# Kernel tuning notes

Hardware: AMD Instinct MI355X
Metric: run time of the kernel (lower is better)

The kernel has to match this reference:

```python
import jax, jax.numpy as jnp
import numpy as np
from jax import lax

NUM_HOP = 2      # opt.num_hop
POOL_HOP = 1     # Encoder(..., num_hop=1) in gnn_pools
K_POOL = 1024    # int(pooling_ratio * num_patches) = 0.5 * 2048
TH = 0.0         # opt.nonzero_th
T = 0.07         # NCE temperature
NEG_FILL = -10.0


def l2norm(x):
    # Normalize(power=2): x / (sum(x^2, dim=1, keepdim)^(1/2))
    return x / jnp.sqrt(jnp.sum(x * x, axis=1, keepdims=True))


def tagconv(A, h, W, b, k):
    # DGL TAGConv: concat_{i=0..k} (D^-1/2 A D^-1/2)^i h, then linear
    deg = jnp.sum(A, axis=1)
    dinv = lax.rsqrt(jnp.maximum(deg, 1e-12))
    An = A * dinv[:, None] * dinv[None, :]   # [N,N] normalized adjacency
    feats = [h]
    for _ in range(k):
        h = An @ h
        feats.append(h)
    return jnp.concatenate(feats, axis=1) @ W + b


def nce_pair(f_t, f_s):
    # calc_gnn NCE: positives = diag(f_t . f_s); negatives = full gram with diag masked to -10
    n = f_t.shape[0]
    eye = jnp.eye(n, dtype=bool)
    pos = jnp.sum(f_t * f_s, axis=1, keepdims=True)          # [N,1]
    neg_s = jnp.where(eye, NEG_FILL, f_t @ f_s.T)            # [N,N]
    neg_t = jnp.where(eye, NEG_FILL, f_s @ f_t.T)
    out_s = jnp.concatenate([pos, neg_s], axis=1) / T
    out_t = jnp.concatenate([pos, neg_t], axis=1) / T
    # CrossEntropy with label 0 == -log_softmax(out)[:, 0], mean over rows
    loss_s = -jnp.mean(jax.nn.log_softmax(out_s, axis=1)[:, 0])
    loss_t = -jnp.mean(jax.nn.log_softmax(out_t, axis=1)[:, 0])
    return loss_s + loss_t


def setup_inputs() -> dict:
    key = jax.random.key(0)
    ks = jax.random.split(key, 8)
    N, C, D = 2048, 512, 128
    g = 0.02  # init_gain ('normal' init)
    return {
        "fs": jax.random.normal(ks[0], (N, C), jnp.float32),
        "ft": jax.random.normal(ks[1], (N, C), jnp.float32),
        "W_embed": g * jax.random.normal(ks[2], (C, D), jnp.float32),
        "b_embed": jnp.zeros((D,), jnp.float32),
        "W_gnn": g * jax.random.normal(ks[3], ((NUM_HOP + 1) * D, D), jnp.float32),
        "b_gnn": jnp.zeros((D,), jnp.float32),
        "W_pool": g * jax.random.normal(ks[4], (D, 1), jnp.float32),
        "b_pool": jnp.zeros((1,), jnp.float32),
        "W_gnnp": g * jax.random.normal(ks[5], ((POOL_HOP + 1) * D, D), jnp.float32),
        "b_gnnp": jnp.zeros((D,), jnp.float32),
    }


def reference(fs, ft, W_embed, b_embed, W_gnn, b_gnn, W_pool, b_pool, W_gnnp, b_gnnp):
    # Embed: linear + l2 norm
    f_es = l2norm(fs @ W_embed + b_embed)   # student [N, nc]
    f_et = l2norm(ft @ W_embed + b_embed)   # teacher [N, nc]

    # nonzero_graph on detached teacher features; same adjacency reused for student
    ft_d = lax.stop_gradient(f_et)
    n = f_et.shape[0]
    eye = jnp.eye(n, dtype=bool)
    A = (ft_d @ ft_d.T > TH).astype(f_et.dtype)
    A = jnp.where(eye, 1.0, A)  # dgl.add_self_loop

    # TAGConv encoder + l2norm; teacher branch detached
    f_gt = lax.stop_gradient(l2norm(tagconv(A, f_et, W_gnn, b_gnn, NUM_HOP)))
    f_gs = l2norm(tagconv(A, f_es, W_gnn, b_gnn, NUM_HOP))
    loss_g = nce_pair(f_gt, f_gs)

    # Pool / top_k_graph
    scores = jax.nn.sigmoid((f_gt @ W_pool + b_pool)[:, 0])   # [N]
    vals, idx = lax.top_k(scores, K_POOL)
    new_ht = f_gt[idx] * vals[:, None]
    new_hs = f_gs[idx] * vals[:, None]
    un = (A > 0).astype(A.dtype)
    un2 = ((un @ un) > 0).astype(A.dtype)        # 2-hop boolean adjacency
    sub = un2[idx][:, idx]                       # [k,k]
    deg = jnp.sum(sub, axis=1)
    g_pool = sub / deg[None, :]                  # replicates torch broadcast in norm_g(g/degrees)

    # pooled-stage Encoder (TAGConv k=1) on the pooled graph structure (with self loops)
    k = K_POOL
    eye_k = jnp.eye(k, dtype=bool)
    Ap = (g_pool > 0).astype(A.dtype)
    Ap = jnp.where(eye_k, 1.0, Ap)
    f_pt = lax.stop_gradient(l2norm(tagconv(Ap, new_ht, W_gnnp, b_gnnp, POOL_HOP)))
    f_ps = l2norm(tagconv(Ap, new_hs, W_gnnp, b_gnnp, POOL_HOP))
    loss_pool = nce_pair(f_pt, f_ps)

    return loss_g + loss_pool
```

## Files before the change

### kernel.cpp

```cpp
#include <hip/hip_runtime.h>


#define TINV (1.0f / 0.07f)

using short8 = __attribute__((ext_vector_type(8))) short;
using f32x4  = __attribute__((ext_vector_type(4))) float;

__device__ __forceinline__ unsigned short f2bf(float f) {
    unsigned u = __float_as_uint(f);
    u += 0x7fff + ((u >> 16) & 1);
    return (unsigned short)(u >> 16);
}

template<bool BT>
__device__ __forceinline__ void mm_tile(const float* __restrict__ A, int lda,
                                        const float* __restrict__ B, int ldb,
                                        int i0, int j0, int k0, int k1,
                                        float (&acc)[4][4],
                                        float (&As)[16][68], float (&Bs)[16][68])
{
    const int tid = threadIdx.x;
    const int tx = tid & 15;
    const int ty = tid >> 4;
    const int lr = tid >> 2;
    const int lc = (tid & 3) * 4;
    for (int k = k0; k < k1; k += 16) {
        float4 av = *(const float4*)(A + (size_t)(i0 + lr) * lda + (k + lc));
        As[lc + 0][lr] = av.x; As[lc + 1][lr] = av.y;
        As[lc + 2][lr] = av.z; As[lc + 3][lr] = av.w;
        if (BT) {
            float4 bv = *(const float4*)(B + (size_t)(j0 + lr) * ldb + (k + lc));
            Bs[lc + 0][lr] = bv.x; Bs[lc + 1][lr] = bv.y;
            Bs[lc + 2][lr] = bv.z; Bs[lc + 3][lr] = bv.w;
        } else {
            const int n = tid & 63;
            const int kb = tid >> 6;
#pragma unroll
            for (int it = 0; it < 4; ++it)
                Bs[kb * 4 + it][n] = B[(size_t)(k + kb * 4 + it) * ldb + (j0 + n)];
        }
        __syncthreads();
#pragma unroll
        for (int kk = 0; kk < 16; ++kk) {
            float a[4], b[4];
#pragma unroll
            for (int u = 0; u < 4; ++u) a[u] = As[kk][ty * 4 + u];
#pragma unroll
            for (int v = 0; v < 4; ++v) b[v] = Bs[kk][tx * 4 + v];
#pragma unroll
            for (int u = 0; u < 4; ++u)
#pragma unroll
                for (int v = 0; v < 4; ++v)
                    acc[u][v] = fmaf(a[u], b[v], acc[u][v]);
        }
        __syncthreads();
    }
}

__device__ __forceinline__ void mm64x128(const unsigned short* __restrict__ Ab, int lda,
                                         const unsigned short* __restrict__ Bb, int ldb,
                                         int i0, int j0, int k0, int Kc,
                                         f32x4 (&acc)[8],
                                         unsigned short (&As)[64][40],
                                         unsigned short (&Bs)[128][40])
{
    const int tid = threadIdx.x;
    const int w = tid >> 6;
    const int lane = tid & 63;
    const int m = lane & 15;
    const int q = lane >> 4;
    const int ar = tid >> 2;
    const int ac = (tid & 3) * 8;
    for (int ks = 0; ks < Kc; ks += 32) {
        const int k = k0 + ks;
        *(ulonglong2*)&As[ar][ac] =
            *(const ulonglong2*)(Ab + (size_t)(i0 + ar) * lda + k + ac);
        *(ulonglong2*)&Bs[ar][ac] =
            *(const ulonglong2*)(Bb + (size_t)(j0 + ar) * ldb + k + ac);
        *(ulonglong2*)&Bs[ar + 64][ac] =
            *(const ulonglong2*)(Bb + (size_t)(j0 + ar + 64) * ldb + k + ac);
        __syncthreads();
        short8 a = *(const short8*)&As[w * 16 + m][q * 8];
#pragma unroll
        for (int nt = 0; nt < 8; ++nt) {
            short8 b = *(const short8*)&Bs[nt * 16 + m][q * 8];
            acc[nt] = __builtin_amdgcn_mfma_f32_16x16x32_bf16(a, b, acc[nt], 0, 0, 0);
        }
        __syncthreads();
    }
}

__launch_bounds__(256)
__global__ void k_setup_embed(const float* __restrict__ fs, const float* __restrict__ ft,
                              const float* __restrict__ W, float* __restrict__ part,
                              size_t zstr, int* __restrict__ zwords, int zcount,
                              float* __restrict__ out,
                              const float* __restrict__ Wg, const float* __restrict__ Wp,
                              unsigned short* __restrict__ Wtall)
{
    __shared__ float As[16][68];
    __shared__ float Bs[16][68];
    const int b = blockIdx.x;
    const int tid = threadIdx.x;
    if (b < 512) {
        const int z = b & 3;
        const int by = (b >> 2) & 63;
        const int bx = b >> 8;
        const float* A = (by < 32) ? ft : fs;
        const int i0 = (by & 31) * 64;
        const int j0 = bx * 64;
        float acc[4][4] = {};
        mm_tile<false>(A, 512, W, 128, i0, j0, z * 128, z * 128 + 128, acc, As, Bs);
        const int tx = tid & 15, ty = tid >> 4;
        float* dst = part + (size_t)z * zstr;
#pragma unroll
        for (int u = 0; u < 4; ++u) {
            const size_t ri = (size_t)(by * 64 + ty * 4 + u) * 128 + j0 + tx * 4;
            float4 vv;
            vv.x = acc[u][0]; vv.y = acc[u][1]; vv.z = acc[u][2]; vv.w = acc[u][3];
            *(float4*)(dst + ri) = vv;
        }
    } else if (b < 561) {
        const int i = (b - 512) * 256 + tid;
        if (i < zcount) zwords[i] = 0;
        if (b == 512 && tid == 0) out[0] = 0.0f;
    } else {
        const int e0 = (b - 561) * 2048 + tid;
#pragma unroll
        for (int it = 0; it < 8; ++it) {
            const int e = e0 + it * 256;
            const int c = e >> 14;
            const int rem = e & 16383;
            const int n = rem >> 7, k = rem & 127;
            const float* src = (c < 3) ? (Wg + (size_t)c * 16384)
                                       : (Wp + (size_t)(c - 3) * 16384);
            Wtall[e] = f2bf(src[(size_t)k * 128 + n]);
        }
    }
}

__global__ void combine_norm(const float* __restrict__ part, int nz, size_t zstr,
                             const float* __restrict__ bias,
                             float* __restrict__ f32out,
                             unsigned short* __restrict__ bf16out)
{
    const int row = blockIdx.x;
    const int tid = threadIdx.x;
    float v = bias[tid];
    for (int z = 0; z < nz; ++z) v += part[(size_t)z * zstr + (size_t)row * 128 + tid];
    __shared__ float red[128];
    red[tid] = v * v;
    __syncthreads();
    for (int s = 64; s > 0; s >>= 1) {
        if (tid < s) red[tid] += red[tid + s];
        __syncthreads();
    }
    const float o = v * (1.0f / sqrtf(red[0]));
    f32out[(size_t)row * 128 + tid] = o;
    bf16out[(size_t)row * 128 + tid] = f2bf(o);
}

__launch_bounds__(256)
__global__ void k_gram_fused(const float* __restrict__ f_e,
                             unsigned short* __restrict__ A01,
                             unsigned long long* __restrict__ bits,
                             int* __restrict__ deg,
                             const unsigned short* __restrict__ feb,
                             const unsigned short* __restrict__ Wt,
                             float* __restrict__ hW)
{
    __shared__ __align__(16) unsigned char smem[15360];
    const int b = blockIdx.x;
    const int tid = threadIdx.x;
    if (b >= 528) {
        unsigned short (&As2)[64][40]  = *reinterpret_cast<unsigned short(*)[64][40]>(smem);
        unsigned short (&Bs2)[128][40] = *reinterpret_cast<unsigned short(*)[128][40]>(smem + 5120);
        const int lb = b - 528;
        const int z = lb >> 6;
        const int i0 = (lb & 63) * 64;
        f32x4 acc[8];
#pragma unroll
        for (int t = 0; t < 8; ++t)
#pragma unroll
            for (int r = 0; r < 4; ++r) acc[t][r] = 0.0f;
        mm64x128(feb, 128, Wt + (size_t)z * 16384, 128, i0, 0, 0, 128, acc, As2, Bs2);
        const int w = tid >> 6, lane = tid & 63, m = lane & 15, q = lane >> 4;
        float* Cb = hW + (size_t)z * (4096ull * 128);
#pragma unroll
        for (int nt = 0; nt < 8; ++nt) {
            const int col = nt * 16 + m;
#pragma unroll
            for (int r = 0; r < 4; ++r) {
                const int row = i0 + w * 16 + q * 4 + r;
                Cb[(size_t)row * 128 + col] = acc[nt][r];
            }
        }
        return;
    }
    float (&As)[16][68] = *reinterpret_cast<float(*)[16][68]>(smem);
    float (&Bs)[16][68] = *reinterpret_cast<float(*)[16][68]>(smem + 4352);
    unsigned char (&nib)[64][16]  = *reinterpret_cast<unsigned char(*)[64][16]>(smem + 8704);
    unsigned char (&nibT)[64][16] = *reinterpret_cast<unsigned char(*)[64][16]>(smem + 9728);
    unsigned long long (&chk)[64]  = *reinterpret_cast<unsigned long long(*)[64]>(smem + 10752);
    unsigned long long (&chkT)[64] = *reinterpret_cast<unsigned long long(*)[64]>(smem + 11264);
    int by = (int)((sqrtf(8.0f * b + 1.0f) - 1.0f) * 0.5f);
    while ((by + 1) * (by + 2) / 2 <= b) ++by;
    while (by * (by + 1) / 2 > b) --by;
    const int bx = b - by * (by + 1) / 2;
    const int i0 = by * 64, j0 = bx * 64;
    float acc[4][4] = {};
    mm_tile<true>(f_e, 128, f_e, 128, i0, j0, 0, 128, acc, As, Bs);
    const int tx = tid & 15, ty = tid >> 4;
    unsigned pb = 0;
#pragma unroll
    for (int u = 0; u < 4; ++u)
#pragma unroll
        for (int v = 0; v < 4; ++v) {
            bool pred = (acc[u][v] > 0.0f) || (i0 + ty * 4 + u == j0 + tx * 4 + v);
            pb |= (unsigned)pred << (u * 4 + v);
        }
#pragma unroll
    for (int u = 0; u < 4; ++u) nib[ty * 4 + u][tx] = (pb >> (4 * u)) & 15;
#pragma unroll
    for (int v = 0; v < 4; ++v) {
        unsigned nt = 0;
#pragma unroll
        for (int u = 0; u < 4; ++u) nt |= ((pb >> (u * 4 + v)) & 1u) << u;
        nibT[tx * 4 + v][ty] = nt;
    }
    __syncthreads();
    if (tid < 64) {
        unsigned long long c = 0;
#pragma unroll
        for (int t = 0; t < 16; ++t) c |= (unsigned long long)nib[tid][t] << (4 * t);
        chk[tid] = c;
        bits[(size_t)(i0 + tid) * 32 + (j0 >> 6)] = c;
        atomicAdd(&deg[i0 + tid], __popcll(c));
    } else if (tid < 128 && bx != by) {
        const int r = tid - 64;
        unsigned long long c = 0;
#pragma unroll
        for (int t = 0; t < 16; ++t) c |= (unsigned long long)nibT[r][t] << (4 * t);
        chkT[r] = c;
        bits[(size_t)(j0 + r) * 32 + (i0 >> 6)] = c;
        atomicAdd(&deg[j0 + r], __popcll(c));
    }
    __syncthreads();
#pragma unroll
    for (int it = 0; it < 4; ++it) {
        const int row = it * 16 + (tid >> 4);
        const int c0 = (tid & 15) * 4;
        unsigned short o[4];
#pragma unroll
        for (int c = 0; c < 4; ++c)
            o[c] = ((chk[row] >> (c0 + c)) & 1) ? (unsigned short)0x3F80 : (unsigned short)0;
        *(ulonglong1*)&A01[(size_t)(i0 + row) * 2048 + j0 + c0] = *(ulonglong1*)o;
        if (bx != by) {
            unsigned short o2[4];
#pragma unroll
            for (int c = 0; c < 4; ++c)
                o2[c] = ((chkT[row] >> (c0 + c)) & 1) ? (unsigned short)0x3F80 : (unsigned short)0;
            *(ulonglong1*)&A01[(size_t)(j0 + row) * 2048 + i0 + c0] = *(ulonglong1*)o2;
        }
    }
}

__launch_bounds__(256)
__global__ void mm_bf16(const unsigned short* __restrict__ A, int lda, size_t aZ,
                        const unsigned short* __restrict__ B, int ldb, size_t bZ,
                        float* __restrict__ C, int ldc, size_t cZ,
                        int Kc, int kZ)
{
    __shared__ unsigned short As[64][40];
    __shared__ unsigned short Bs[128][40];
    const int tid = threadIdx.x;
    const int bz = blockIdx.z;
    const int i0 = blockIdx.y * 64;
    const int j0 = blockIdx.x * 128;
    const int k0 = bz * kZ;
    const unsigned short* Ab = A + (size_t)bz * aZ;
    const unsigned short* Bb = B + (size_t)bz * bZ;
    float* Cb = C + (size_t)bz * cZ;
    f32x4 acc[8];
#pragma unroll
    for (int t = 0; t < 8; ++t)
#pragma unroll
        for (int r = 0; r < 4; ++r) acc[t][r] = 0.0f;
    mm64x128(Ab, lda, Bb, ldb, i0, j0, k0, Kc, acc, As, Bs);
    const int w = tid >> 6, lane = tid & 63, m = lane & 15, q = lane >> 4;
#pragma unroll
    for (int nt = 0; nt < 8; ++nt) {
        const int col = j0 + nt * 16 + m;
#pragma unroll
        for (int r = 0; r < 4; ++r) {
            const int row = i0 + w * 16 + q * 4 + r;
            Cb[(size_t)row * ldc + col] = acc[nt][r];
        }
    }
}

__global__ void reduce_xt(const float* __restrict__ part, int nz, size_t zstr,
                          int M, const float* __restrict__ dinv,
                          const float* __restrict__ addT,
                          unsigned short* __restrict__ xt)
{
    __shared__ float T[32][33];
    const int tid = threadIdx.x;
    const int iloc = tid >> 3, nq = (tid & 7) * 4;
    const int n = blockIdx.x * 32 + nq;
    const int i = blockIdx.y * 32 + iloc;
    float4 s = *(const float4*)(part + (size_t)i * 256 + n);
    for (int z = 1; z < nz; ++z) {
        float4 t = *(const float4*)(part + (size_t)z * zstr + (size_t)i * 256 + n);
        s.x += t.x; s.y += t.y; s.z += t.z; s.w += t.w;
    }
    const float d = dinv[i];
    const int srow = (n >= 128 ? M : 0) + i;
    float4 a = *(const float4*)(addT + (size_t)srow * 128 + (n & 127));
    T[nq + 0][iloc] = (a.x + s.x * d) * d;
    T[nq + 1][iloc] = (a.y + s.y * d) * d;
    T[nq + 2][iloc] = (a.z + s.z * d) * d;
    T[nq + 3][iloc] = (a.w + s.w * d) * d;
    __syncthreads();
    const int nloc = tid >> 3, ic = (tid & 7) * 4;
    unsigned short o2[4];
#pragma unroll
    for (int c = 0; c < 4; ++c) o2[c] = f2bf(T[nloc][ic + c]);
    *(ulonglong1*)(xt + (size_t)(blockIdx.x * 32 + nloc) * M + blockIdx.y * 32 + ic) =
        *(ulonglong1*)o2;
}

__global__ void combine_tag(const float* __restrict__ part, int nz, size_t zstr,
                            int Mnodes,
                            const float* __restrict__ add,
                            const float* __restrict__ dinv,
                            const float* __restrict__ bias,
                            float* __restrict__ f32out,
                            unsigned short* __restrict__ bf16out,
                            const float* __restrict__ Wp, const float* __restrict__ bp,
                            float* __restrict__ scores)
{
    const int row = blockIdx.x;
    const int tid = threadIdx.x;
    const int node = (row < Mnodes) ? row : row - Mnodes;
    const int boff = (row < Mnodes) ? 0 : 128;
    float s = 0.0f;
    for (int z = 0; z < nz; ++z)
        s += part[(size_t)z * zstr + (size_t)node * 256 + boff + tid];
    float v = bias[tid] + add[(size_t)row * 128 + tid] + dinv[node] * s;
    __shared__ float red[128];
    red[tid] = v * v;
    __syncthreads();
    for (int st = 64; st > 0; st >>= 1) {
        if (tid < st) red[tid] += red[tid + st];
        __syncthreads();
    }
    const float o = v * (1.0f / sqrtf(red[0]));
    if (f32out) f32out[(size_t)row * 128 + tid] = o;
    bf16out[(size_t)row * 128 + tid] = f2bf(o);
    if (Wp && row < Mnodes) {
        __syncthreads();
        red[tid] = o * Wp[tid];
        __syncthreads();
        for (int st = 64; st > 0; st >>= 1) {
            if (tid < st) red[tid] += red[tid + st];
            __syncthreads();
        }
        if (tid == 0) scores[row] = 1.0f / (1.0f + expf(-(red[0] + bp[0])));
    }
}

__global__ void make_xt(const float* __restrict__ src, const int* __restrict__ deg,
                        unsigned short* __restrict__ xt, float* __restrict__ dinv)
{
    __shared__ float T[32][33];
    const int b = blockIdx.x;
    const int bx = b & 7, by = b >> 3;
    const int tid = threadIdx.x;
    const int iloc = tid >> 3, nq = (tid & 7) * 4;
    const int n0 = bx * 32;
    const int i = by * 32 + iloc;
    const int srow = (n0 >= 128 ? 2048 : 0) + i;
    float4 f = *(const float4*)(src + (size_t)srow * 128 + ((n0 + nq) & 127));
    const float d = 1.0f / sqrtf((float)deg[i]);
    if (bx == 0 && (tid & 7) == 0) dinv[i] = d;
    T[nq + 0][iloc] = f.x * d; T[nq + 1][iloc] = f.y * d;
    T[nq + 2][iloc] = f.z * d; T[nq + 3][iloc] = f.w * d;
    __syncthreads();
    const int nloc = tid >> 3, ic = (tid & 7) * 4;
    unsigned short o[4];
#pragma unroll
    for (int c = 0; c < 4; ++c) o[c] = f2bf(T[nloc][ic + c]);
    *(ulonglong1*)(xt + (size_t)(n0 + nloc) * 2048 + by * 32 + ic) = *(ulonglong1*)o;
}

__launch_bounds__(256)
__global__ void k_nce_topk(const unsigned short* __restrict__ A,
                           const unsigned short* __restrict__ B,
                           float* __restrict__ rowsum, float* __restrict__ colsum,
                           float* __restrict__ pos, int gramBlocks, int bw,
                           const float* __restrict__ scores,
                           float* __restrict__ vals, int* __restrict__ idx)
{
    __shared__ unsigned short As[64][40];
    __shared__ unsigned short Bs[128][40];
    __shared__ float colbuf[4][128];
    __shared__ unsigned sv[2048];
    __shared__ int hist[256];
    __shared__ int shp, shr, sh_base, sh_out, wsum[5];
    const int tid = threadIdx.x;
    const int b = blockIdx.x;
    if (b < gramBlocks) {
        const int bx = b % bw, by = b / bw;
        const int i0 = by * 64;
        const int j0 = bx * 128;
        const int w = tid >> 6;
        const int lane = tid & 63;
        const int m = lane & 15;
        const int q = lane >> 4;
        f32x4 acc[8];
#pragma unroll
        for (int t = 0; t < 8; ++t)
#pragma unroll
            for (int r = 0; r < 4; ++r) acc[t][r] = 0.0f;
        mm64x128(A, 128, B, 128, i0, j0, 0, 128, acc, As, Bs);
        float rpart[4] = {0.0f, 0.0f, 0.0f, 0.0f};
        float cpart[8];
#pragma unroll
        for (int nt = 0; nt < 8; ++nt) {
            const int col = j0 + nt * 16 + m;
            float cs = 0.0f;
#pragma unroll
            for (int r = 0; r < 4; ++r) {
                const int row = i0 + w * 16 + q * 4 + r;
                float g = acc[nt][r];
                float e = __expf(g * TINV);
                if (row == col) { pos[row] = g; e = 0.0f; }
                rpart[r] += e;
                cs += e;
            }
            cpart[nt] = cs;
        }
#pragma unroll
        for (int r = 0; r < 4; ++r) {
            float v = rpart[r];
            v += __shfl_xor(v, 1); v += __shfl_xor(v, 2);
            v += __shfl_xor(v, 4); v += __shfl_xor(v, 8);
            if (m == 0) atomicAdd(&rowsum[i0 + w * 16 + q * 4 + r], v);
        }
#pragma unroll
        for (int nt = 0; nt < 8; ++nt) {
            float v = cpart[nt];
            v += __shfl_xor(v, 16); v += __shfl_xor(v, 32);
            if (q == 0) colbuf[w][nt * 16 + m] = v;
        }
        __syncthreads();
        if (tid < 128) {
            float v = colbuf[0][tid] + colbuf[1][tid] + colbuf[2][tid] + colbuf[3][tid];
            atomicAdd(&colsum[j0 + tid], v);
        }
    } else {
        for (int e = tid; e < 2048; e += 256) sv[e] = __float_as_uint(scores[e]);
        if (tid == 0) { shp = 0; shr = 1024; sh_base = 0; sh_out = 0; }
        __syncthreads();
        for (int byte = 3; byte >= 0; --byte) {
            hist[tid] = 0;
            __syncthreads();
            const unsigned pref = (unsigned)shp;
            const unsigned pmask = (byte == 3) ? 0u : (0xFFFFFFFFu << ((byte + 1) * 8));
            for (int e = tid; e < 2048; e += 256) {
                unsigned u = sv[e];
                if ((u & pmask) == (pref & pmask))
                    atomicAdd(&hist[(u >> (byte * 8)) & 255], 1);
            }
            __syncthreads();
            if (tid == 0) {
                int rem = shr, bs = 255;
                for (; bs > 0; --bs) {
                    if (hist[bs] >= rem) break;
                    rem -= hist[bs];
                }
                shp = (int)(pref | ((unsigned)bs << (byte * 8)));
                shr = rem;
            }
            __syncthreads();
        }
        const unsigned t = (unsigned)shp;
        const int remain = shr;
        const int lane = tid & 63, wave = tid >> 6;
        for (int pass = 0; pass < 8; ++pass) {
            const int e = pass * 256 + tid;
            const unsigned u = sv[e];
            const bool eq = (u == t);
            unsigned long long mk = __ballot(eq);
            int wpre = __popcll(mk & ((1ull << lane) - 1ull));
            if (lane == 0) wsum[wave] = __popcll(mk);
            __syncthreads();
            if (tid == 0) {
                int a = sh_base;
                for (int ww = 0; ww < 4; ++ww) { int c = wsum[ww]; wsum[ww] = a; a += c; }
                sh_base = a;
            }
            __syncthreads();
            const int rank = eq ? (wsum[wave] + wpre) : 0x7fffffff;
            if ((u > t) || (eq && rank < remain)) {
                int slot = atomicAdd(&sh_out, 1);
                idx[slot] = e;
                vals[slot] = __uint_as_float(u);
            }
            __syncthreads();
        }
    }
}

__global__ void k_final_ap(const float* __restrict__ rs, const float* __restrict__ cs,
                           const float* __restrict__ pos, float* __restrict__ out,
                           const unsigned long long* __restrict__ bits,
                           const int* __restrict__ idx,
                           unsigned short* __restrict__ Ap, int* __restrict__ degp)
{
    __shared__ unsigned long long pb[32][33];
    __shared__ unsigned long long qb[32][33];
    __shared__ float red[256];
    const int b = blockIdx.x;
    const int tid = threadIdx.x;
    if (b < 1024) {
        const int tp = (b >> 5) * 32;
        const int tq = (b & 31) * 32;
        for (int t = tid; t < 1024; t += 256) {
            int r = t >> 5, w = t & 31;
            pb[r][w] = bits[(size_t)idx[tp + r] * 32 + w];
            qb[r][w] = bits[(size_t)idx[tq + r] * 32 + w];
        }
        __syncthreads();
        const int pi = tid >> 3;
        const int qc0 = (tid & 7) * 4;
        unsigned long long a0 = 0, a1 = 0, a2 = 0, a3 = 0;
#pragma unroll
        for (int w = 0; w < 32; ++w) {
            const unsigned long long p = pb[pi][w];
            a0 |= p & qb[qc0 + 0][w];
            a1 |= p & qb[qc0 + 1][w];
            a2 |= p & qb[qc0 + 2][w];
            a3 |= p & qb[qc0 + 3][w];
        }
        unsigned short o[4] = { (unsigned short)(a0 ? 0x3F80 : 0),
                                (unsigned short)(a1 ? 0x3F80 : 0),
                                (unsigned short)(a2 ? 0x3F80 : 0),
                                (unsigned short)(a3 ? 0x3F80 : 0) };
        *(ulonglong1*)&Ap[(size_t)(tp + pi) * 1024 + tq + qc0] = *(ulonglong1*)o;
        int v = (a0 ? 1 : 0) + (a1 ? 1 : 0) + (a2 ? 1 : 0) + (a3 ? 1 : 0);
        v += __shfl_xor(v, 1); v += __shfl_xor(v, 2); v += __shfl_xor(v, 4);
        if ((tid & 7) == 0) atomicAdd(&degp[tp + pi], v);
    } else {
        const int i = (b - 1024) * 256 + tid;
        float p = pos[i] * TINV;
        float ep = __expf(p);
        float t = (logf(rs[i] + ep) - p) + (logf(cs[i] + ep) - p);
        red[tid] = t;
        __syncthreads();
        for (int s = 128; s > 0; s >>= 1) {
            if (tid < s) red[tid] += red[tid + s];
            __syncthreads();
        }
        if (tid == 0) atomicAdd(out, red[0] * (1.0f / 2048.0f));
    }
}

__global__ void nce_final(const float* __restrict__ rs, const float* __restrict__ cs,
                          const float* __restrict__ pos, float invN,
                          float* __restrict__ out)
{
    const int i = blockIdx.x * 256 + threadIdx.x;
    float p = pos[i] * TINV;
    float ep = __expf(p);
    float t = (logf(rs[i] + ep) - p) + (logf(cs[i] + ep) - p);
    __shared__ float red[256];
    red[threadIdx.x] = t;
    __syncthreads();
    for (int s = 128; s > 0; s >>= 1) {
        if (threadIdx.x < s) red[threadIdx.x] += red[threadIdx.x + s];
        __syncthreads();
    }
    if (threadIdx.x == 0) atomicAdd(out, red[0] * invN);
}

__global__ void gather_nh(const float* __restrict__ f_g, const int* __restrict__ idx,
                          const float* __restrict__ vals, const int* __restrict__ degp,
                          unsigned short* __restrict__ nhb, float* __restrict__ dinvp)
{
    const int b = blockIdx.x;
    const int tid = threadIdx.x;
    if (b < 4) {
        const int p2 = b * 256 + tid;
        dinvp[p2] = 1.0f / sqrtf((float)degp[p2]);
    }
    const int hrow = b * 8 + (tid >> 5);
    const int cq = (tid & 31) * 4;
    const int p = hrow & 1023;
    const int s = idx[p];
    const float v = vals[p];
    const int srow = (hrow >= 1024 ? 2048 : 0) + s;
    float4 f = *(const float4*)(f_g + (size_t)srow * 128 + cq);
    unsigned short o[4] = { f2bf(f.x * v), f2bf(f.y * v), f2bf(f.z * v), f2bf(f.w * v) };
    *(ulonglong1*)&nhb[(size_t)hrow * 128 + cq] = *(ulonglong1*)o;
}

__launch_bounds__(256)
__global__ void k_lin_pool(const unsigned short* __restrict__ nhb,
                           const unsigned short* __restrict__ WtP,
                           const float* __restrict__ dinvp,
                           float* __restrict__ P0,
                           unsigned short* __restrict__ Xtp)
{
    __shared__ unsigned short As[64][40];
    __shared__ unsigned short Bs[128][40];
    const int b = blockIdx.x;
    const int z = b >> 5;
    const int i0 = (b & 31) * 64;
    const int tid = threadIdx.x;
    f32x4 acc[8];
#pragma unroll
    for (int t = 0; t < 8; ++t)
#pragma unroll
        for (int r = 0; r < 4; ++r) acc[t][r] = 0.0f;
    mm64x128(nhb, 128, WtP + (size_t)z * 16384, 128, i0, 0, 0, 128, acc, As, Bs);
    const int w = tid >> 6, lane = tid & 63, m = lane & 15, q = lane >> 4;
    if (z == 0) {
#pragma unroll
        for (int nt = 0; nt < 8; ++nt) {
            const int col = nt * 16 + m;
#pragma unroll
            for (int r = 0; r < 4; ++r) {
                const int row = i0 + w * 16 + q * 4 + r;
                P0[(size_t)row * 128 + col] = acc[nt][r];
            }
        }
    } else {
        const int boff = (i0 >= 1024) ? 128 : 0;
        const int p0 = (i0 & 1023) + w * 16 + q * 4;
        float4 dv = *(const float4*)(dinvp + p0);
        const float dvr[4] = { dv.x, dv.y, dv.z, dv.w };
#pragma unroll
        for (int nt = 0; nt < 8; ++nt) {
            const int n = boff + nt * 16 + m;
            unsigned short o[4];
#pragma unroll
            for (int r = 0; r < 4; ++r) o[r] = f2bf(acc[nt][r] * dvr[r]);
            *(ulonglong1*)&Xtp[(size_t)n * 1024 + p0] = *(ulonglong1*)o;
        }
    }
}

extern "C" void kernel_launch(void* const* d_in, const int* in_sizes, int n_in,
                              void* d_out, int out_size, void* d_ws, size_t ws_size,
                              hipStream_t stream)
{
    (void)in_sizes; (void)n_in; (void)out_size; (void)ws_size;
    const float* fs      = (const float*)d_in[0];
    const float* ft      = (const float*)d_in[1];
    const float* W_embed = (const float*)d_in[2];
    const float* b_embed = (const float*)d_in[3];
    const float* W_gnn   = (const float*)d_in[4];
    const float* b_gnn   = (const float*)d_in[5];
    const float* W_pool  = (const float*)d_in[6];
    const float* b_pool  = (const float*)d_in[7];
    const float* W_gnnp  = (const float*)d_in[8];
    const float* b_gnnp  = (const float*)d_in[9];
    float* out = (float*)d_out;

    float* ws = (float*)d_ws;
    size_t o = 0;
    auto alloc = [&](size_t n) { float* p = ws + o; o += (n + 3) & ~3ull; return p; };
    float* bigB   = alloc(2048ull * 2048);
    float* f_e    = alloc(4096 * 128);
    float* f_g    = alloc(4096 * 128);
    unsigned short* A01  = (unsigned short*)alloc(2048ull * 2048 / 2);
    unsigned short* feb  = (unsigned short*)alloc(4096ull * 128 / 2);
    unsigned short* Xt1  = (unsigned short*)alloc(256ull * 2048 / 2);
    unsigned short* Xt2  = (unsigned short*)alloc(256ull * 2048 / 2);
    unsigned short* f_gb = (unsigned short*)alloc(4096ull * 128 / 2);
    unsigned short* Wtall= (unsigned short*)alloc(5ull * 16384 / 2);
    unsigned short* Ap01 = (unsigned short*)alloc(1024ull * 1024 / 2);
    unsigned short* nhb  = (unsigned short*)alloc(2048ull * 128 / 2);
    unsigned short* Xtp  = (unsigned short*)alloc(256ull * 1024 / 2);
    unsigned short* f_pb = (unsigned short*)alloc(2048ull * 128 / 2);
    float* hW     = alloc(3ull * 4096 * 128);
    float* P0     = alloc(2048ull * 128);
    float* dinv   = alloc(2048);
    float* scores = alloc(2048);
    float* vals   = alloc(1024);
    int*   idxb   = (int*)alloc(1024);
    float* dinvp  = alloc(1024);
    unsigned long long* bits = (unsigned long long*)alloc(2048 * 32 * 2);
    float* nceb = alloc(9216);
    int*   deg  = (int*)alloc(2048);
    int*   degp = (int*)alloc(1024);
    const int kZeroCount = 9216 + 2048 + 1024;

    const size_t FSTR = 4096ull * 128;
    const size_t PSTR = 1024ull * 256;
    unsigned short* Wt  = Wtall;
    unsigned short* WtP = Wtall + 3ull * 16384;
    float* hW0 = hW;
    float* hW1 = hW + FSTR;
    float* hW2 = hW + 2 * FSTR;
    float* rs  = nceb;
    float* csu = nceb + 2048;
    float* pos = nceb + 4096;
    float* rsp  = nceb + 6144;
    float* csp  = nceb + 7168;
    float* posp = nceb + 8192;

    k_setup_embed<<<601, 256, 0, stream>>>(fs, ft, W_embed, bigB, FSTR,
                                           (int*)nceb, kZeroCount, out, W_gnn, W_gnnp, Wtall);
    combine_norm<<<4096, 128, 0, stream>>>(bigB, 4, FSTR, b_embed, f_e, feb);
    k_gram_fused<<<720, 256, 0, stream>>>(f_e, A01, bits, deg, feb, Wt, hW);
    make_xt<<<512, 256, 0, stream>>>(hW2, deg, Xt1, dinv);
    mm_bf16<<<dim3(2, 32, 4), 256, 0, stream>>>(A01, 2048, 0, Xt1, 2048, 0,
                                                bigB, 256, FSTR, 512, 512);
    reduce_xt<<<dim3(8, 64), 256, 0, stream>>>(bigB, 4, FSTR, 2048, dinv, hW1, Xt2);
    mm_bf16<<<dim3(2, 32, 4), 256, 0, stream>>>(A01, 2048, 0, Xt2, 2048, 0,
                                                bigB, 256, FSTR, 512, 512);
    combine_tag<<<4096, 128, 0, stream>>>(bigB, 4, FSTR, 2048, hW0, dinv, b_gnn,
                                          f_g, f_gb, W_pool, b_pool, scores);
    k_nce_topk<<<513, 256, 0, stream>>>(f_gb, f_gb + 2048 * 128, rs, csu, pos,
                                        512, 16, scores, vals, idxb);
    k_final_ap<<<1032, 256, 0, stream>>>(rs, csu, pos, out, bits, idxb, Ap01, degp);
    gather_nh<<<256, 256, 0, stream>>>(f_g, idxb, vals, degp, nhb, dinvp);
    k_lin_pool<<<64, 256, 0, stream>>>(nhb, WtP, dinvp, P0, Xtp);
    mm_bf16<<<dim3(2, 16, 4), 256, 0, stream>>>(Ap01, 1024, 0, Xtp, 1024, 0,
                                                bigB, 256, PSTR, 256, 256);
    combine_tag<<<2048, 128, 0, stream>>>(bigB, 4, PSTR, 1024, P0, dinvp, b_gnnp,
                                          nullptr, f_pb, nullptr, nullptr, nullptr);
    k_nce_topk<<<128, 256, 0, stream>>>(f_pb, f_pb + 1024 * 128, rsp, csp, posp,
                                        128, 8, nullptr, nullptr, nullptr);
    nce_final<<<4, 256, 0, stream>>>(rsp, csp, posp, 1.0f / 1024.0f, out);
}
```

Before: 208.3 us.

## Replace FP32 SIMT GEMMs with split-bf16 MFMA in embed and gram kernels

The embedding GEMM and the gram/adjacency GEMM now run on MFMA bf16 matrix instructions. Each fp32 operand is split into high and low bf16 parts and three products are accumulated (hh, hl, lh) to keep close to fp32 accuracy, which matters for the sign threshold. This replaces the scalar FMA tile loops and drops the fp32 f_e buffer in favour of hi/lo bf16 copies. The cost is extra conversion work and LDS traffic, a larger shared-memory footprint, and slight numerical differences that could flip near-zero adjacency entries.

```diff
diff --git a/kernel.cpp b/kernel.cpp
--- a/kernel.cpp
+++ b/kernel.cpp
@@ -11,50 +11,12 @@
     u += 0x7fff + ((u >> 16) & 1);
     return (unsigned short)(u >> 16);
 }
-
-template<bool BT>
-__device__ __forceinline__ void mm_tile(const float* __restrict__ A, int lda,
-                                        const float* __restrict__ B, int ldb,
-                                        int i0, int j0, int k0, int k1,
-                                        float (&acc)[4][4],
-                                        float (&As)[16][68], float (&Bs)[16][68])
-{
-    const int tid = threadIdx.x;
-    const int tx = tid & 15;
-    const int ty = tid >> 4;
-    const int lr = tid >> 2;
-    const int lc = (tid & 3) * 4;
-    for (int k = k0; k < k1; k += 16) {
-        float4 av = *(const float4*)(A + (size_t)(i0 + lr) * lda + (k + lc));
-        As[lc + 0][lr] = av.x; As[lc + 1][lr] = av.y;
-        As[lc + 2][lr] = av.z; As[lc + 3][lr] = av.w;
-        if (BT) {
-            float4 bv = *(const float4*)(B + (size_t)(j0 + lr) * ldb + (k + lc));
-            Bs[lc + 0][lr] = bv.x; Bs[lc + 1][lr] = bv.y;
-            Bs[lc + 2][lr] = bv.z; Bs[lc + 3][lr] = bv.w;
-        } else {
-            const int n = tid & 63;
-            const int kb = tid >> 6;
-#pragma unroll
-            for (int it = 0; it < 4; ++it)
-                Bs[kb * 4 + it][n] = B[(size_t)(k + kb * 4 + it) * ldb + (j0 + n)];
-        }
-        __syncthreads();
-#pragma unroll
-        for (int kk = 0; kk < 16; ++kk) {
-            float a[4], b[4];
-#pragma unroll
-            for (int u = 0; u < 4; ++u) a[u] = As[kk][ty * 4 + u];
-#pragma unroll
-            for (int v = 0; v < 4; ++v) b[v] = Bs[kk][tx * 4 + v];
-#pragma unroll
-            for (int u = 0; u < 4; ++u)
-#pragma unroll
-                for (int v = 0; v < 4; ++v)
-                    acc[u][v] = fmaf(a[u], b[v], acc[u][v]);
-        }
-        __syncthreads();
-    }
+__device__ __forceinline__ float bf2f(unsigned short h) {
+    return __uint_as_float((unsigned)h << 16);
+}
+__device__ __forceinline__ void splitbf(float f, unsigned short& h, unsigned short& l) {
+    h = f2bf(f);
+    l = f2bf(f - bf2f(h));
 }
 
 __device__ __forceinline__ void mm64x128(const unsigned short* __restrict__ Ab, int lda,
@@ -98,34 +60,79 @@
                               const float* __restrict__ Wg, const float* __restrict__ Wp,
                               unsigned short* __restrict__ Wtall)
 {
-    __shared__ float As[16][68];
-    __shared__ float Bs[16][68];
+    __shared__ unsigned short Ah[64][40];
+    __shared__ unsigned short Al[64][40];
+    __shared__ unsigned short Bh[128][40];
+    __shared__ unsigned short Bl[128][40];
     const int b = blockIdx.x;
     const int tid = threadIdx.x;
-    if (b < 512) {
+    if (b < 256) {
         const int z = b & 3;
-        const int by = (b >> 2) & 63;
-        const int bx = b >> 8;
-        const float* A = (by < 32) ? ft : fs;
-        const int i0 = (by & 31) * 64;
-        const int j0 = bx * 64;
-        float acc[4][4] = {};
-        mm_tile<false>(A, 512, W, 128, i0, j0, z * 128, z * 128 + 128, acc, As, Bs);
-        const int tx = tid & 15, ty = tid >> 4;
+        const int my = b >> 2;
+        const float* A = (my < 32) ? ft : fs;
+        const int i0 = (my & 31) * 64;
+        const int w = tid >> 6, lane = tid & 63, m = lane & 15, q = lane >> 4;
+        const int ar = tid >> 2, ac = (tid & 3) * 8;
+        const int wkk = tid >> 3, wc0 = (tid & 7) * 16;
+        f32x4 acc[8];
+#pragma unroll
+        for (int t = 0; t < 8; ++t)
+#pragma unroll
+            for (int r = 0; r < 4; ++r) acc[t][r] = 0.0f;
+        for (int ks = 0; ks < 128; ks += 32) {
+            const int k = z * 128 + ks;
+            {
+                float4 f1 = *(const float4*)(A + (size_t)(i0 + ar) * 512 + k + ac);
+                float4 f2 = *(const float4*)(A + (size_t)(i0 + ar) * 512 + k + ac + 4);
+                unsigned short h[8], l[8];
+                splitbf(f1.x, h[0], l[0]); splitbf(f1.y, h[1], l[1]);
+                splitbf(f1.z, h[2], l[2]); splitbf(f1.w, h[3], l[3]);
+                splitbf(f2.x, h[4], l[4]); splitbf(f2.y, h[5], l[5]);
+                splitbf(f2.z, h[6], l[6]); splitbf(f2.w, h[7], l[7]);
+#pragma unroll
+                for (int j = 0; j < 8; ++j) { Ah[ar][ac + j] = h[j]; Al[ar][ac + j] = l[j]; }
+            }
+            {
+                const float* Wr = W + (size_t)(k + wkk) * 128 + wc0;
+#pragma unroll
+                for (int jj = 0; jj < 4; ++jj) {
+                    float4 f = *(const float4*)(Wr + jj * 4);
+                    unsigned short h, l;
+                    splitbf(f.x, h, l); Bh[wc0 + jj*4 + 0][wkk] = h; Bl[wc0 + jj*4 + 0][wkk] = l;
+                    splitbf(f.y, h, l); Bh[wc0 + jj*4 + 1][wkk] = h; Bl[wc0 + jj*4 + 1][wkk] = l;
+                    splitbf(f.z, h, l); Bh[wc0 + jj*4 + 2][wkk] = h; Bl[wc0 + jj*4 + 2][wkk] = l;
+                    splitbf(f.w, h, l); Bh[wc0 + jj*4 + 3][wkk] = h; Bl[wc0 + jj*4 + 3][wkk] = l;
+                }
+            }
+            __syncthreads();
+            short8 ah = *(const short8*)&Ah[w * 16 + m][q * 8];
+            short8 al = *(const short8*)&Al[w * 16 + m][q * 8];
+#pragma unroll
+            for (int nt = 0; nt < 8; ++nt) {
+                short8 bh = *(const short8*)&Bh[nt * 16 + m][q * 8];
+                short8 bl = *(const short8*)&Bl[nt * 16 + m][q * 8];
+                acc[nt] = __builtin_amdgcn_mfma_f32_16x16x32_bf16(ah, bh, acc[nt], 0, 0, 0);
+                acc[nt] = __builtin_amdgcn_mfma_f32_16x16x32_bf16(ah, bl, acc[nt], 0, 0, 0);
+                acc[nt] = __builtin_amdgcn_mfma_f32_16x16x32_bf16(al, bh, acc[nt], 0, 0, 0);
+            }
+            __syncthreads();
+        }
         float* dst = part + (size_t)z * zstr;
 #pragma unroll
-        for (int u = 0; u < 4; ++u) {
-            const size_t ri = (size_t)(by * 64 + ty * 4 + u) * 128 + j0 + tx * 4;
-            float4 vv;
-            vv.x = acc[u][0]; vv.y = acc[u][1]; vv.z = acc[u][2]; vv.w = acc[u][3];
-            *(float4*)(dst + ri) = vv;
-        }
-    } else if (b < 561) {
-        const int i = (b - 512) * 256 + tid;
+        for (int nt = 0; nt < 8; ++nt) {
+            const int col = nt * 16 + m;
+#pragma unroll
+            for (int r = 0; r < 4; ++r) {
+                const int row = my * 64 + w * 16 + q * 4 + r;
+                dst[(size_t)row * 128 + col] = acc[nt][r];
+            }
+        }
+    } else if (b < 305) {
+        const int i = (b - 256) * 256 + tid;
         if (i < zcount) zwords[i] = 0;
-        if (b == 512 && tid == 0) out[0] = 0.0f;
+        if (b == 256 && tid == 0) out[0] = 0.0f;
     } else {
-        const int e0 = (b - 561) * 2048 + tid;
+        const int e0 = (b - 305) * 2048 + tid;
 #pragma unroll
         for (int it = 0; it < 8; ++it) {
             const int e = e0 + it * 256;
@@ -141,8 +148,8 @@
 
 __global__ void combine_norm(const float* __restrict__ part, int nz, size_t zstr,
                              const float* __restrict__ bias,
-                             float* __restrict__ f32out,
-                             unsigned short* __restrict__ bf16out)
+                             unsigned short* __restrict__ bfh,
+                             unsigned short* __restrict__ bfl)
 {
     const int row = blockIdx.x;
     const int tid = threadIdx.x;
@@ -156,20 +163,22 @@
         __syncthreads();
     }
     const float o = v * (1.0f / sqrtf(red[0]));
-    f32out[(size_t)row * 128 + tid] = o;
-    bf16out[(size_t)row * 128 + tid] = f2bf(o);
+    unsigned short h, l;
+    splitbf(o, h, l);
+    bfh[(size_t)row * 128 + tid] = h;
+    bfl[(size_t)row * 128 + tid] = l;
 }
 
 __launch_bounds__(256)
-__global__ void k_gram_fused(const float* __restrict__ f_e,
+__global__ void k_gram_fused(const unsigned short* __restrict__ febh,
+                             const unsigned short* __restrict__ febl,
                              unsigned short* __restrict__ A01,
                              unsigned long long* __restrict__ bits,
                              int* __restrict__ deg,
-                             const unsigned short* __restrict__ feb,
                              const unsigned short* __restrict__ Wt,
                              float* __restrict__ hW)
 {
-    __shared__ __align__(16) unsigned char smem[15360];
+    __shared__ __align__(16) unsigned char smem[25600];
     const int b = blockIdx.x;
     const int tid = threadIdx.x;
     if (b >= 528) {
@@ -183,7 +192,7 @@
         for (int t = 0; t < 8; ++t)
 #pragma unroll
             for (int r = 0; r < 4; ++r) acc[t][r] = 0.0f;
-        mm64x128(feb, 128, Wt + (size_t)z * 16384, 128, i0, 0, 0, 128, acc, As2, Bs2);
+        mm64x128(febh, 128, Wt + (size_t)z * 16384, 128, i0, 0, 0, 128, acc, As2, Bs2);
         const int w = tid >> 6, lane = tid & 63, m = lane & 15, q = lane >> 4;
         float* Cb = hW + (size_t)z * (4096ull * 128);
 #pragma unroll
@@ -197,42 +206,65 @@
         }
         return;
     }
-    float (&As)[16][68] = *reinterpret_cast<float(*)[16][68]>(smem);
-    float (&Bs)[16][68] = *reinterpret_cast<float(*)[16][68]>(smem + 4352);
-    unsigned char (&nib)[64][16]  = *reinterpret_cast<unsigned char(*)[64][16]>(smem + 8704);
-    unsigned char (&nibT)[64][16] = *reinterpret_cast<unsigned char(*)[64][16]>(smem + 9728);
-    unsigned long long (&chk)[64]  = *reinterpret_cast<unsigned long long(*)[64]>(smem + 10752);
-    unsigned long long (&chkT)[64] = *reinterpret_cast<unsigned long long(*)[64]>(smem + 11264);
+    unsigned short (&Ah)[64][40] = *reinterpret_cast<unsigned short(*)[64][40]>(smem);
+    unsigned short (&Al)[64][40] = *reinterpret_cast<unsigned short(*)[64][40]>(smem + 5120);
+    unsigned short (&Bh)[64][40] = *reinterpret_cast<unsigned short(*)[64][40]>(smem + 10240);
+    unsigned short (&Bl)[64][40] = *reinterpret_cast<unsigned short(*)[64][40]>(smem + 15360);
+    unsigned char (&predB)[64][64] = *reinterpret_cast<unsigned char(*)[64][64]>(smem + 20480);
+    unsigned long long (&chk)[64]  = *reinterpret_cast<unsigned long long(*)[64]>(smem + 24576);
+    unsigned long long (&chkT)[64] = *reinterpret_cast<unsigned long long(*)[64]>(smem + 25088);
     int by = (int)((sqrtf(8.0f * b + 1.0f) - 1.0f) * 0.5f);
     while ((by + 1) * (by + 2) / 2 <= b) ++by;
     while (by * (by + 1) / 2 > b) --by;
     const int bx = b - by * (by + 1) / 2;
     const int i0 = by * 64, j0 = bx * 64;
-    float acc[4][4] = {};
-    mm_tile<true>(f_e, 128, f_e, 128, i0, j0, 0, 128, acc, As, Bs);
-    const int tx = tid & 15, ty = tid >> 4;
-    unsigned pb = 0;
-#pragma unroll
-    for (int u = 0; u < 4; ++u)
-#pragma unroll
-        for (int v = 0; v < 4; ++v) {
-            bool pred = (acc[u][v] > 0.0f) || (i0 + ty * 4 + u == j0 + tx * 4 + v);
-            pb |= (unsigned)pred << (u * 4 + v);
-        }
-#pragma unroll
-    for (int u = 0; u < 4; ++u) nib[ty * 4 + u][tx] = (pb >> (4 * u)) & 15;
-#pragma unroll
-    for (int v = 0; v < 4; ++v) {
-        unsigned nt = 0;
-#pragma unroll
-        for (int u = 0; u < 4; ++u) nt |= ((pb >> (u * 4 + v)) & 1u) << u;
-        nibT[tx * 4 + v][ty] = nt;
+    const int w = tid >> 6, lane = tid & 63, m = lane & 15, q = lane >> 4;
+    const int ar = tid >> 2, ac = (tid & 3) * 8;
+    f32x4 acc[4];
+#pragma unroll
+    for (int t = 0; t < 4; ++t)
+#pragma unroll
+        for (int r = 0; r < 4; ++r) acc[t][r] = 0.0f;
+    for (int ks = 0; ks < 128; ks += 32) {
+        *(ulonglong2*)&Ah[ar][ac] = *(const ulonglong2*)(febh + (size_t)(i0 + ar) * 128 + ks + ac);
+        *(ulonglong2*)&Al[ar][ac] = *(const ulonglong2*)(febl + (size_t)(i0 + ar) * 128 + ks + ac);
+        *(ulonglong2*)&Bh[ar][ac] = *(const ulonglong2*)(febh + (size_t)(j0 + ar) * 128 + ks + ac);
+        *(ulonglong2*)&Bl[ar][ac] = *(const ulonglong2*)(febl + (size_t)(j0 + ar) * 128 + ks + ac);
+        __syncthreads();
+        short8 ah = *(const short8*)&Ah[w * 16 + m][q * 8];
+        short8 al = *(const short8*)&Al[w * 16 + m][q * 8];
+#pragma unroll
+        for (int nt = 0; nt < 4; ++nt) {
+            short8 bh = *(const short8*)&Bh[nt * 16 + m][q * 8];
+            short8 bl = *(const short8*)&Bl[nt * 16 + m][q * 8];
+            acc[nt] = __builtin_amdgcn_mfma_f32_16x16x32_bf16(ah, bh, acc[nt], 0, 0, 0);
+            acc[nt] = __builtin_amdgcn_mfma_f32_16x16x32_bf16(ah, bl, acc[nt], 0, 0, 0);
+            acc[nt] = __builtin_amdgcn_mfma_f32_16x16x32_bf16(al, bh, acc[nt], 0, 0, 0);
+        }
+        __syncthreads();
+    }
+#pragma unroll
+    for (int nt = 0; nt < 4; ++nt) {
+        const int lc = nt * 16 + m;
+#pragma unroll
+        for (int r = 0; r < 4; ++r) {
+            const int lr = w * 16 + q * 4 + r;
+            bool pred = (acc[nt][r] > 0.0f) || (i0 + lr == j0 + lc);
+            predB[lr][lc] = pred ? 1 : 0;
+        }
     }
     __syncthreads();
     if (tid < 64) {
         unsigned long long c = 0;
-#pragma unroll
-        for (int t = 0; t < 16; ++t) c |= (unsigned long long)nib[tid][t] << (4 * t);
+        const unsigned* rowp = (const unsigned*)predB[tid];
+#pragma unroll
+        for (int t = 0; t < 16; ++t) {
+            unsigned u = rowp[t];
+            c |= (unsigned long long)((u >> 0) & 1) << (4 * t + 0);
+            c |= (unsigned long long)((u >> 8) & 1) << (4 * t + 1);
+            c |= (unsigned long long)((u >> 16) & 1) << (4 * t + 2);
+            c |= (unsigned long long)((u >> 24) & 1) << (4 * t + 3);
+        }
         chk[tid] = c;
         bits[(size_t)(i0 + tid) * 32 + (j0 >> 6)] = c;
         atomicAdd(&deg[i0 + tid], __popcll(c));
@@ -240,7 +272,8 @@
         const int r = tid - 64;
         unsigned long long c = 0;
 #pragma unroll
-        for (int t = 0; t < 16; ++t) c |= (unsigned long long)nibT[r][t] << (4 * t);
+        for (int i = 0; i < 64; ++i)
+            c |= (unsigned long long)(predB[i][r] & 1) << i;
         chkT[r] = c;
         bits[(size_t)(j0 + r) * 32 + (i0 >> 6)] = c;
         atomicAdd(&deg[j0 + r], __popcll(c));
@@ -673,10 +706,10 @@
     size_t o = 0;
     auto alloc = [&](size_t n) { float* p = ws + o; o += (n + 3) & ~3ull; return p; };
     float* bigB   = alloc(2048ull * 2048);
-    float* f_e    = alloc(4096 * 128);
     float* f_g    = alloc(4096 * 128);
     unsigned short* A01  = (unsigned short*)alloc(2048ull * 2048 / 2);
     unsigned short* feb  = (unsigned short*)alloc(4096ull * 128 / 2);
+    unsigned short* febl = (unsigned short*)alloc(4096ull * 128 / 2);
     unsigned short* Xt1  = (unsigned short*)alloc(256ull * 2048 / 2);
     unsigned short* Xt2  = (unsigned short*)alloc(256ull * 2048 / 2);
     unsigned short* f_gb = (unsigned short*)alloc(4096ull * 128 / 2);
@@ -712,10 +745,10 @@
     float* csp  = nceb + 7168;
     float* posp = nceb + 8192;
 
-    k_setup_embed<<<601, 256, 0, stream>>>(fs, ft, W_embed, bigB, FSTR,
+    k_setup_embed<<<345, 256, 0, stream>>>(fs, ft, W_embed, bigB, FSTR,
                                            (int*)nceb, kZeroCount, out, W_gnn, W_gnnp, Wtall);
-    combine_norm<<<4096, 128, 0, stream>>>(bigB, 4, FSTR, b_embed, f_e, feb);
-    k_gram_fused<<<720, 256, 0, stream>>>(f_e, A01, bits, deg, feb, Wt, hW);
+    combine_norm<<<4096, 128, 0, stream>>>(bigB, 4, FSTR, b_embed, feb, febl);
+    k_gram_fused<<<720, 256, 0, stream>>>(feb, febl, A01, bits, deg, Wt, hW);
     make_xt<<<512, 256, 0, stream>>>(hW2, deg, Xt1, dinv);
     mm_bf16<<<dim3(2, 32, 4), 256, 0, stream>>>(A01, 2048, 0, Xt1, 2048, 0,
                                                 bigB, 256, FSTR, 512, 512);
```

After: 201.6 us (median of 2 runs). -3.2%, faster.
